# Optimization experiments

Measured on AMD Instinct MI355X. Metric: run time of the kernel, lower is better.

## Reference

```python
import jax, jax.numpy as jnp
import numpy as np
from jax import lax

NHEAD = 8
DC = 32
BN_EPS = 1e-5


def setup_inputs() -> dict:
    key = jax.random.key(0)
    ks = jax.random.split(key, 8)
    b, t, h, w = 8, 128, 32, 64
    l = h * w
    prev_attn = jax.random.uniform(ks[0], (b * NHEAD, t, l), dtype=jnp.float32)
    curr_attn = jax.random.uniform(ks[1], (b * NHEAD, t, l), dtype=jnp.float32)
    key_padding_mask = jax.random.bernoulli(ks[2], 0.2, (b, l))  # True = padded
    conv_w = jax.random.normal(ks[3], (DC, 2 * NHEAD, 5, 5), dtype=jnp.float32) * 0.05
    conv_b = jnp.zeros((DC,), dtype=jnp.float32)
    proj_w = jax.random.normal(ks[4], (NHEAD, DC, 1, 1), dtype=jnp.float32) * 0.1
    bn_gamma = jnp.ones((NHEAD,), dtype=jnp.float32)
    bn_beta = jnp.zeros((NHEAD,), dtype=jnp.float32)
    return {"prev_attn": prev_attn, "curr_attn": curr_attn,
            "key_padding_mask": key_padding_mask, "h": 32,
            "conv_w": conv_w, "conv_b": conv_b, "proj_w": proj_w,
            "bn_gamma": bn_gamma, "bn_beta": bn_beta}


def _forward(prev_attn, curr_attn, conv_w, conv_b, proj_w, bn_gamma, bn_beta,
             key_padding_mask, h):
    b, l = key_padding_mask.shape
    t = curr_attn.shape[1]
    w = l // h
    n = NHEAD
    prev = prev_attn.reshape(b, n, t, l)
    curr = curr_attn.reshape(b, n, t, l)
    attns = jnp.concatenate([prev, curr], axis=1)            # (b, 2n, t, l)
    attns = jnp.cumsum(attns, axis=2) - attns                # exclusive cumsum over t
    # 'b n t (h w) -> (b t) n h w'
    attns = attns.transpose(0, 2, 1, 3).reshape(b * t, 2 * n, h, w)
    cov = lax.conv_general_dilated(attns, conv_w, (1, 1), [(2, 2), (2, 2)],
                                   dimension_numbers=("NCHW", "OIHW", "NCHW"))
    cov = jax.nn.relu(cov + conv_b[None, :, None, None])
    # mask: 'b (h w) -> (b t) 1 h w'
    mask = jnp.broadcast_to(key_padding_mask.reshape(b, 1, 1, h, w),
                            (b, t, 1, h, w)).reshape(b * t, 1, h, w)
    cov = jnp.where(mask, 0.0, cov)
    # 1x1 conv, no bias
    cov = jnp.einsum("bdhw,nd->bnhw", cov, proj_w[:, :, 0, 0])  # (bt, n, h, w)
    # MaskBatchNorm2d: BN over unmasked pixels (training-mode batch stats)
    nm = (~mask).astype(cov.dtype)                              # (bt, 1, h, w)
    cnt = jnp.maximum(nm.sum(), 1.0)
    mean = (cov * nm).sum(axis=(0, 2, 3)) / cnt                 # (n,)
    diff = cov - mean[None, :, None, None]
    var = (diff * diff * nm).sum(axis=(0, 2, 3)) / cnt          # biased var
    y = bn_gamma[None, :, None, None] * diff * lax.rsqrt(var + BN_EPS)[None, :, None, None] \
        + bn_beta[None, :, None, None]
    cov = jnp.where(mask, cov, y)
    # '(b t) n h w -> (b n) t (h w)'
    cov = cov.reshape(b, t, n, h * w).transpose(0, 2, 1, 3).reshape(b * n, t, h * w)
    return cov


def reference(prev_attn, curr_attn, key_padding_mask, h,
              conv_w, conv_b, proj_w, bn_gamma, bn_beta):
    return _forward(prev_attn, curr_attn, conv_w, conv_b, proj_w,
                    bn_gamma, bn_beta, key_padding_mask, h)
```

## Files before the change

kernel.cpp:

```cpp
#include <hip/hip_runtime.h>
#include <hip/hip_bf16.h>


typedef __attribute__((ext_vector_type(4))) float f32x4;
typedef __attribute__((ext_vector_type(8))) short short8;
typedef __attribute__((ext_vector_type(8))) unsigned short u16x8;

#define B_   8
#define NH   8
#define T_   128
#define H_   32
#define W_   64
#define L_   2048
#define CIN  16
#define DCC  32
#define WSTR 420

__device__ __forceinline__ unsigned short f2h(float f){
  _Float16 h = (_Float16)f;
  return __builtin_bit_cast(unsigned short, h);
}
__device__ __forceinline__ float h2f(unsigned short u){
  _Float16 h = __builtin_bit_cast(_Float16, u);
  return (float)h;
}
__device__ __forceinline__ int swz(int a){ return a ^ ((a >> 3) & 0x30); }

__global__ void k_cumsum(const float* __restrict__ prev,
                         const float* __restrict__ curr,
                         uint2* __restrict__ cum2)
{
  int gid = blockIdx.x * 256 + threadIdx.x;
  int p4 = gid & 511;
  int ci = (gid >> 9) & 15;
  int b  = gid >> 13;
  const float* src = ((ci < 8)
      ? prev + ((size_t)(b*8 + ci) * T_) * L_
      : curr + ((size_t)(b*8 + ci - 8) * T_) * L_) + p4*4;
  uint2* dst = cum2 + ((size_t)(b*CIN + ci) * T_) * (L_/4) + p4;
  float a0 = 0.f, a1 = 0.f, a2 = 0.f, a3 = 0.f;
  #pragma unroll 4
  for (int t = 0; t < T_; t++){
    uint2 o;
    o.x = (unsigned)f2h(a0) | ((unsigned)f2h(a1) << 16);
    o.y = (unsigned)f2h(a2) | ((unsigned)f2h(a3) << 16);
    dst[(size_t)t * (L_/4)] = o;
    f32x4 v = *(const f32x4*)(src + (size_t)t * L_);
    a0 += v.x; a1 += v.y; a2 += v.z; a3 += v.w;
  }
}

__global__ void k_prep(const float* __restrict__ convw,
                       const float* __restrict__ projw,
                       const void* __restrict__ mraw,
                       unsigned short* __restrict__ Wt,
                       unsigned short* __restrict__ Pt,
                       unsigned char* __restrict__ mB,
                       float* __restrict__ cntOut)
{
  int tid = threadIdx.x;
  int blk = blockIdx.x;
  if (blk < 32){
    int co = blk;
    for (int k = tid; k < WSTR; k += 256){
      float v = 0.f;
      if (k < 400){
        int tap = k >> 4, ci = k & 15;
        int dy = tap / 5, dx = tap - dy*5;
        v = convw[(((co*CIN + ci)*5 + dy)*5) + dx];
      }
      Wt[co*WSTR + k] = f2h(v);
    }
  } else if (blk == 32){
    for (int idx = tid; idx < 16*32; idx += 256){
      int n = idx >> 5, q = idx & 31;
      float v = (n < 8) ? projw[n*32 + 16*(q & 1) + (q >> 1)] : 0.f;
      Pt[idx] = f2h(v);
    }
  } else {
    __shared__ int s_flags;
    __shared__ int s_cnt;
    if (tid == 0){ s_flags = 0; s_cnt = 0; }
    __syncthreads();
    const unsigned* w = (const unsigned*)mraw;
    int fl = 0;
    for (int i = tid; i < 4096; i += 256){
      unsigned v = w[i];
      if (v == 0x3F800000u) fl |= 2;
      else if (v > 1u)      fl |= 1;
      else if (v == 1u)     fl |= 4;
    }
    if (fl) atomicOr(&s_flags, fl);
    __syncthreads();
    int flags = s_flags;
    int mode = (flags & 1) ? 0 : ((flags & 2) ? 2 : ((flags & 4) ? 1 : 0));
    int c = 0;
    int base = (blk - 33) * 1024;
    for (int k = 0; k < 4; k++){
      int i = base + k*256 + tid;
      int m;
      if (mode == 0)      m = (((const unsigned char*)mraw)[i] != 0);
      else if (mode == 2) m = (((const float*)mraw)[i] != 0.f);
      else                m = (((const int*)mraw)[i] != 0);
      mB[i] = (unsigned char)m;
      c += 1 - m;
    }
    atomicAdd(&s_cnt, c);
    __syncthreads();
    if (tid == 0) atomicAdd(cntOut, 128.0f * (float)s_cnt);
  }
}

__global__ __launch_bounds__(256, 3) void k_conv(
    const unsigned short* __restrict__ cumIn,
    const unsigned short* __restrict__ Wt,
    const unsigned short* __restrict__ Pt,
    const unsigned char* __restrict__ mB,
    const float* __restrict__ convb,
    unsigned short* __restrict__ cov,
    float* __restrict__ slots)
{
  __shared__ alignas(16) unsigned short img[20*68*16];
  __shared__ alignas(16) unsigned short plds[16*32];
  __shared__ alignas(16) unsigned sval[4][16*20];
  __shared__ unsigned long long mbl[16];

  const int tid  = threadIdx.x;
  const int bid  = blockIdx.x;
  const int half = bid & 1;
  const int bt   = bid >> 1;
  const int t    = bt & 127;
  const int b    = bt >> 7;
  const int ylo  = half * 16;
  const int lane = tid & 63;
  const int wv   = tid >> 6;
  const int mrow = lane & 15;
  const int kb   = lane >> 4;

  if (wv == 0){
    #pragma unroll
    for (int k2 = 0; k2 < 16; k2++){
      int m = mB[b*L_ + half*1024 + k2*64 + lane];
      unsigned long long bal = __ballot(m != 0);
      if (lane == 0) mbl[k2] = bal;
    }
  } else if (wv == 1){
    const uint4* srcp = (const uint4*)Pt;
    uint4* dstp = (uint4*)plds;
    if (lane < 64) { for (int i = lane; i < 64; i += 64) dstp[i] = srcp[i]; }
  }

  for (int it = tid; it < 640; it += 256){
    int cp  = it & 7;
    int xxi = (it >> 3) & 3;
    int yy  = it >> 5;
    int xx  = (xxi < 2) ? xxi : 64 + xxi;
    int ad  = ((yy*68 + xx)*16 + 2*cp)*2;
    *(unsigned*)((char*)img + swz(ad)) = 0u;
  }
  #pragma unroll
  for (int iter = 0; iter < 5; iter++){
    int it = iter*256 + tid;
    int xc = it & 7;
    int cp = (it >> 3) & 7;
    int yy = it >> 6;
    int y  = ylo - 2 + yy;
    u16x8 v0 = (u16x8)0, v1 = (u16x8)0;
    if (y >= 0 && y < H_){
      const unsigned short* r0 = cumIn + (((size_t)(b*CIN + 2*cp) * T_ + t) * L_) + y*W_ + xc*8;
      v0 = *(const u16x8*)r0;
      v1 = *(const u16x8*)(r0 + (size_t)T_ * L_);
    }
    int sbase = ((yy*68 + 2 + xc*8)*16 + 2*cp)*2;
    #pragma unroll
    for (int j = 0; j < 8; j++){
      unsigned wd = (unsigned)v0[j] | ((unsigned)v1[j] << 16);
      int ad = sbase + j*32;
      *(unsigned*)((char*)img + swz(ad)) = wd;
    }
  }
  __syncthreads();

  const float cb0 = convb[mrow];
  const float cb1 = convb[mrow + 16];
  const short8 pbf = *(const short8*)&plds[mrow*32 + kb*8];
  const unsigned short* Wg = Wt + mrow*WSTR + kb*8;

  int offs_[13];
  #pragma unroll
  for (int ks = 0; ks < 13; ks++){
    int tap = ks*2 + (kb >> 1);
    if (tap > 24) tap = 24;
    int dy = tap / 5, dx = tap - dy*5;
    offs_[ks] = (dy*68 + dx)*32 + (kb & 1)*16;
  }

  float ssum = 0.f, ssq = 0.f;

  #pragma unroll 1
  for (int c = 0; c < 2; c++){
    int wofs = 0;
    asm volatile("" : "+v"(wofs));
    const int pbase = wv*256 + c*128;
    const unsigned long long mw0 = mbl[(pbase >> 6)];
    const unsigned long long mw1 = mbl[(pbase >> 6) + 1];
    const int base_u = ((pbase >> 6)*68 + mrow)*32;
    f32x4 acc[8][2];
    #pragma unroll
    for (int mt = 0; mt < 8; mt++){ acc[mt][0] = (f32x4)0.f; acc[mt][1] = (f32x4)0.f; }

    #pragma unroll
    for (int ks = 0; ks < 13; ks++){
      short8 bfa = *(const short8*)(Wg + wofs + ks*32);
      short8 bfb = *(const short8*)(Wg + wofs + 6720 + ks*32);
      const char* p0 = (const char*)img + swz(base_u + offs_[ks]);
      const char* p1 = (const char*)img + swz(base_u + 2176 + offs_[ks]);
      short8 a[8];
      a[0] = *(const short8*)(p0);
      a[1] = *(const short8*)(p0 + 512);
      a[2] = *(const short8*)(p0 + 1024);
      a[3] = *(const short8*)(p0 + 1536);
      a[4] = *(const short8*)(p1);
      a[5] = *(const short8*)(p1 + 512);
      a[6] = *(const short8*)(p1 + 1024);
      a[7] = *(const short8*)(p1 + 1536);
      __builtin_amdgcn_s_setprio(1);
      #pragma unroll
      for (int mt = 0; mt < 8; mt++){
        acc[mt][0] = __builtin_amdgcn_mfma_f32_16x16x32_f16(a[mt], bfa, acc[mt][0], 0, 0, 0);
        acc[mt][1] = __builtin_amdgcn_mfma_f32_16x16x32_f16(a[mt], bfb, acc[mt][1], 0, 0, 0);
      }
      __builtin_amdgcn_s_setprio(0);
    }

    unsigned* sv = &sval[wv][0];
    #pragma unroll
    for (int mt = 0; mt <= 8; mt++){
      if (mt >= 1){
        const int m = mt - 1;
        short8 pa = *(const short8*)&sv[mrow*20 + kb*4];
        f32x4 pc = (f32x4)0.f;
        pc = __builtin_amdgcn_mfma_f32_16x16x32_f16(pa, pbf, pc, 0, 0, 0);
        if (mrow < 8){
          const unsigned long long mwm = (m < 4) ? mw0 : mw1;
          size_t covbase = (((size_t)bt*NH + mrow) * L_) + half*1024 + pbase + m*16 + kb*4;
          uint2 st;
          st.x = (unsigned)f2h(pc[0]) | ((unsigned)f2h(pc[1]) << 16);
          st.y = (unsigned)f2h(pc[2]) | ((unsigned)f2h(pc[3]) << 16);
          *(uint2*)&cov[covbase] = st;
          #pragma unroll
          for (int r = 0; r < 4; r++){
            int bi = (m*16 + kb*4 + r) & 63;
            if (!((mwm >> bi) & 1)){ ssum += pc[r]; ssq += pc[r]*pc[r]; }
          }
        }
      }
      if (mt < 8){
        const unsigned long long mw = (mt < 4) ? mw0 : mw1;
        #pragma unroll
        for (int r = 0; r < 4; r++){
          int bi  = (mt*16 + kb*4 + r) & 63;
          int msk = (int)((mw >> bi) & 1);
          float v0 = fmaxf(acc[mt][0][r] + cb0, 0.f);
          float v1 = fmaxf(acc[mt][1][r] + cb1, 0.f);
          if (msk){ v0 = 0.f; v1 = 0.f; }
          unsigned pd = (unsigned)f2h(v0) | ((unsigned)f2h(v1) << 16);
          sv[(kb*4 + r)*20 + mrow] = pd;
        }
      }
    }
  }

  ssum += __shfl_xor(ssum, 16);
  ssum += __shfl_xor(ssum, 32);
  ssq  += __shfl_xor(ssq, 16);
  ssq  += __shfl_xor(ssq, 32);
  if (lane < 8){
    atomicAdd(&slots[(bid & 7)*16 + lane],     ssum);
    atomicAdd(&slots[(bid & 7)*16 + 8 + lane], ssq);
  }
}

__global__ void k_stats(const float* __restrict__ slots,
                        const float* __restrict__ cntp,
                        const float* __restrict__ gamma,
                        const float* __restrict__ beta,
                        float* __restrict__ ab)
{
  int tid = threadIdx.x;
  if (tid < 8){
    double s = 0.0, q = 0.0;
    for (int i = 0; i < 8; i++){
      s += (double)slots[i*16 + tid];
      q += (double)slots[i*16 + 8 + tid];
    }
    double cnt  = (double)fmaxf(*cntp, 1.0f);
    double mean = s / cnt;
    double var  = q / cnt - mean*mean;
    float inv = (float)(1.0 / sqrt(var + 1e-5));
    float A = gamma[tid] * inv;
    float Bc = beta[tid] - (float)mean * A;
    ab[tid]     = A;
    ab[8 + tid] = Bc;
  }
}

__global__ void k_out(const unsigned short* __restrict__ cov,
                      const unsigned char* __restrict__ mB,
                      const float* __restrict__ ab,
                      float* __restrict__ out)
{
  size_t gid = (size_t)blockIdx.x * 256 + threadIdx.x;
  size_t e = gid * 8;
  int px = (int)(e & 2047);
  size_t r = e >> 11;
  int t = (int)(r & 127); r >>= 7;
  int n = (int)(r & 7);
  int b = (int)(r >> 3);
  const unsigned short* cp = cov + ((((size_t)b*T_ + t)*NH + n) << 11) + px;
  u16x8 cv = *(const u16x8*)cp;
  unsigned long long mm = *(const unsigned long long*)(mB + (size_t)b*L_ + px);
  float A = ab[n], Bc = ab[8 + n];
  float res[8];
  #pragma unroll
  for (int j = 0; j < 8; j++){
    float v = h2f(cv[j]);
    res[j] = ((mm >> (8*j)) & 0xFFull) ? v : (A*v + Bc);
  }
  f32x4* o = (f32x4*)(out + e);
  o[0] = (f32x4){res[0], res[1], res[2], res[3]};
  o[1] = (f32x4){res[4], res[5], res[6], res[7]};
}

extern "C" void kernel_launch(void* const* d_in, const int* in_sizes, int n_in,
                              void* d_out, int out_size, void* d_ws, size_t ws_size,
                              hipStream_t stream)
{
  const float* prev  = (const float*)d_in[0];
  const float* curr  = (const float*)d_in[1];
  const void*  mraw  = d_in[2];
  const float* convw = (const float*)d_in[4];
  const float* convb = (const float*)d_in[5];
  const float* projw = (const float*)d_in[6];
  const float* gamma = (const float*)d_in[7];
  const float* beta  = (const float*)d_in[8];
  float* out = (float*)d_out;

  char* ws = (char*)d_ws;
  unsigned short* cumIn = (unsigned short*)(ws);
  unsigned short* cov   = (unsigned short*)(ws + 67108864);
  unsigned char*  mB    = (unsigned char*) (ws + 100663296);
  unsigned short* Wt    = (unsigned short*)(ws + 100679680);
  unsigned short* Pt    = (unsigned short*)(ws + 100706560);
  float* slots          = (float*)(ws + 100707584);
  float* cntp           = (float*)(ws + 100708096);
  float* ab             = (float*)(ws + 100708160);
  if (ws_size < (size_t)100708224) return;

  hipMemsetAsync(slots, 0, 640, stream);
  k_prep  <<<49,   256, 0, stream>>>(convw, projw, mraw, Wt, Pt, mB, cntp);
  k_cumsum<<<256,  256, 0, stream>>>(prev, curr, (uint2*)cumIn);
  k_conv  <<<2048, 256, 0, stream>>>(cumIn, Wt, Pt, mB, convb, cov, slots);
  k_stats <<<1,    64,  0, stream>>>(slots, cntp, gamma, beta, ab);
  k_out   <<<8192, 256, 0, stream>>>(cov, mB, ab, out);
}
```

Baseline: 179.6 us.

## Double-buffer conv fragment loads, batch staging loads, widen cumsum parallelism

In the conv kernel the LDS A-fragments and weight B-fragments for the next tap step are now loaded ahead of the current step's MFMAs (software prefetch), so LDS latency can overlap with matrix math. The global loads for the image tile are all issued before any LDS stores, giving more memory-level parallelism. The cumsum kernel processes 2 columns per thread instead of 4 and launches twice as many blocks, adding parallelism to the strided scan at the cost of narrower memory accesses. The prefetch raises register pressure, which may reduce occupancy.

```diff
diff --git a/kernel.cpp b/kernel.cpp
--- a/kernel.cpp
+++ b/kernel.cpp
@@ -3,6 +3,7 @@
 
 
 typedef __attribute__((ext_vector_type(4))) float f32x4;
+typedef __attribute__((ext_vector_type(2))) float f32x2;
 typedef __attribute__((ext_vector_type(8))) short short8;
 typedef __attribute__((ext_vector_type(8))) unsigned short u16x8;
 
@@ -28,25 +29,22 @@
 
 __global__ void k_cumsum(const float* __restrict__ prev,
                          const float* __restrict__ curr,
-                         uint2* __restrict__ cum2)
+                         unsigned* __restrict__ cum1)
 {
   int gid = blockIdx.x * 256 + threadIdx.x;
-  int p4 = gid & 511;
-  int ci = (gid >> 9) & 15;
-  int b  = gid >> 13;
+  int p2 = gid & 1023;
+  int ci = (gid >> 10) & 15;
+  int b  = gid >> 14;
   const float* src = ((ci < 8)
       ? prev + ((size_t)(b*8 + ci) * T_) * L_
-      : curr + ((size_t)(b*8 + ci - 8) * T_) * L_) + p4*4;
-  uint2* dst = cum2 + ((size_t)(b*CIN + ci) * T_) * (L_/4) + p4;
-  float a0 = 0.f, a1 = 0.f, a2 = 0.f, a3 = 0.f;
-  #pragma unroll 4
+      : curr + ((size_t)(b*8 + ci - 8) * T_) * L_) + p2*2;
+  unsigned* dst = cum1 + ((size_t)(b*CIN + ci) * T_) * (L_/2) + p2;
+  float a0 = 0.f, a1 = 0.f;
+  #pragma unroll 8
   for (int t = 0; t < T_; t++){
-    uint2 o;
-    o.x = (unsigned)f2h(a0) | ((unsigned)f2h(a1) << 16);
-    o.y = (unsigned)f2h(a2) | ((unsigned)f2h(a3) << 16);
-    dst[(size_t)t * (L_/4)] = o;
-    f32x4 v = *(const f32x4*)(src + (size_t)t * L_);
-    a0 += v.x; a1 += v.y; a2 += v.z; a3 += v.w;
+    dst[(size_t)t * (L_/2)] = (unsigned)f2h(a0) | ((unsigned)f2h(a1) << 16);
+    f32x2 v = *(const f32x2*)(src + (size_t)t * L_);
+    a0 += v.x; a1 += v.y;
   }
 }
 
@@ -147,7 +145,7 @@
   } else if (wv == 1){
     const uint4* srcp = (const uint4*)Pt;
     uint4* dstp = (uint4*)plds;
-    if (lane < 64) { for (int i = lane; i < 64; i += 64) dstp[i] = srcp[i]; }
+    for (int i = lane; i < 64; i += 64) dstp[i] = srcp[i];
   }
 
   for (int it = tid; it < 640; it += 256){
@@ -158,25 +156,31 @@
     int ad  = ((yy*68 + xx)*16 + 2*cp)*2;
     *(unsigned*)((char*)img + swz(ad)) = 0u;
   }
-  #pragma unroll
-  for (int iter = 0; iter < 5; iter++){
-    int it = iter*256 + tid;
-    int xc = it & 7;
-    int cp = (it >> 3) & 7;
-    int yy = it >> 6;
-    int y  = ylo - 2 + yy;
-    u16x8 v0 = (u16x8)0, v1 = (u16x8)0;
-    if (y >= 0 && y < H_){
-      const unsigned short* r0 = cumIn + (((size_t)(b*CIN + 2*cp) * T_ + t) * L_) + y*W_ + xc*8;
-      v0 = *(const u16x8*)r0;
-      v1 = *(const u16x8*)(r0 + (size_t)T_ * L_);
-    }
-    int sbase = ((yy*68 + 2 + xc*8)*16 + 2*cp)*2;
-    #pragma unroll
-    for (int j = 0; j < 8; j++){
-      unsigned wd = (unsigned)v0[j] | ((unsigned)v1[j] << 16);
-      int ad = sbase + j*32;
-      *(unsigned*)((char*)img + swz(ad)) = wd;
+  {
+    u16x8 sv0[5], sv1[5];
+    int sb_[5];
+    #pragma unroll
+    for (int iter = 0; iter < 5; iter++){
+      int it = iter*256 + tid;
+      int xc = it & 7;
+      int cp = (it >> 3) & 7;
+      int yy = it >> 6;
+      int y  = ylo - 2 + yy;
+      sv0[iter] = (u16x8)0; sv1[iter] = (u16x8)0;
+      if (y >= 0 && y < H_){
+        const unsigned short* r0 = cumIn + (((size_t)(b*CIN + 2*cp) * T_ + t) * L_) + y*W_ + xc*8;
+        sv0[iter] = *(const u16x8*)r0;
+        sv1[iter] = *(const u16x8*)(r0 + (size_t)T_ * L_);
+      }
+      sb_[iter] = ((yy*68 + 2 + xc*8)*16 + 2*cp)*2;
+    }
+    #pragma unroll
+    for (int iter = 0; iter < 5; iter++){
+      #pragma unroll
+      for (int j = 0; j < 8; j++){
+        unsigned wd = (unsigned)sv0[iter][j] | ((unsigned)sv1[iter][j] << 16);
+        *(unsigned*)((char*)img + swz(sb_[iter] + j*32)) = wd;
+      }
     }
   }
   __syncthreads();
@@ -185,6 +189,7 @@
   const float cb1 = convb[mrow + 16];
   const short8 pbf = *(const short8*)&plds[mrow*32 + kb*8];
   const unsigned short* Wg = Wt + mrow*WSTR + kb*8;
+  const char* imgc = (const char*)img;
 
   int offs_[13];
   #pragma unroll
@@ -209,21 +214,41 @@
     #pragma unroll
     for (int mt = 0; mt < 8; mt++){ acc[mt][0] = (f32x4)0.f; acc[mt][1] = (f32x4)0.f; }
 
+    short8 nbfa = *(const short8*)(Wg + wofs);
+    short8 nbfb = *(const short8*)(Wg + wofs + 6720);
+    short8 an[8];
+    {
+      const char* p0 = imgc + swz(base_u + offs_[0]);
+      const char* p1 = imgc + swz(base_u + 2176 + offs_[0]);
+      an[0] = *(const short8*)(p0);
+      an[1] = *(const short8*)(p0 + 512);
+      an[2] = *(const short8*)(p0 + 1024);
+      an[3] = *(const short8*)(p0 + 1536);
+      an[4] = *(const short8*)(p1);
+      an[5] = *(const short8*)(p1 + 512);
+      an[6] = *(const short8*)(p1 + 1024);
+      an[7] = *(const short8*)(p1 + 1536);
+    }
     #pragma unroll
     for (int ks = 0; ks < 13; ks++){
-      short8 bfa = *(const short8*)(Wg + wofs + ks*32);
-      short8 bfb = *(const short8*)(Wg + wofs + 6720 + ks*32);
-      const char* p0 = (const char*)img + swz(base_u + offs_[ks]);
-      const char* p1 = (const char*)img + swz(base_u + 2176 + offs_[ks]);
+      short8 bfa = nbfa, bfb = nbfb;
       short8 a[8];
-      a[0] = *(const short8*)(p0);
-      a[1] = *(const short8*)(p0 + 512);
-      a[2] = *(const short8*)(p0 + 1024);
-      a[3] = *(const short8*)(p0 + 1536);
-      a[4] = *(const short8*)(p1);
-      a[5] = *(const short8*)(p1 + 512);
-      a[6] = *(const short8*)(p1 + 1024);
-      a[7] = *(const short8*)(p1 + 1536);
+      #pragma unroll
+      for (int i = 0; i < 8; i++) a[i] = an[i];
+      if (ks < 12){
+        nbfa = *(const short8*)(Wg + wofs + (ks+1)*32);
+        nbfb = *(const short8*)(Wg + wofs + 6720 + (ks+1)*32);
+        const char* p0 = imgc + swz(base_u + offs_[ks+1]);
+        const char* p1 = imgc + swz(base_u + 2176 + offs_[ks+1]);
+        an[0] = *(const short8*)(p0);
+        an[1] = *(const short8*)(p0 + 512);
+        an[2] = *(const short8*)(p0 + 1024);
+        an[3] = *(const short8*)(p0 + 1536);
+        an[4] = *(const short8*)(p1);
+        an[5] = *(const short8*)(p1 + 512);
+        an[6] = *(const short8*)(p1 + 1024);
+        an[7] = *(const short8*)(p1 + 1536);
+      }
       __builtin_amdgcn_s_setprio(1);
       #pragma unroll
       for (int mt = 0; mt < 8; mt++){
@@ -359,7 +384,7 @@
 
   hipMemsetAsync(slots, 0, 640, stream);
   k_prep  <<<49,   256, 0, stream>>>(convw, projw, mraw, Wt, Pt, mB, cntp);
-  k_cumsum<<<256,  256, 0, stream>>>(prev, curr, (uint2*)cumIn);
+  k_cumsum<<<512,  256, 0, stream>>>(prev, curr, (unsigned*)cumIn);
   k_conv  <<<2048, 256, 0, stream>>>(cumIn, Wt, Pt, mB, convb, cov, slots);
   k_stats <<<1,    64,  0, stream>>>(slots, cntp, gamma, beta, ab);
   k_out   <<<8192, 256, 0, stream>>>(cov, mB, ab, out);
```

After: 203.4 us. +13.2%, slower.
